# Kernel tuning notes

Measured on AMD Instinct MI355X. Metric: run time of the kernel, lower is better.

The kernel has to match this reference:

```python
import jax, jax.numpy as jnp
import numpy as np

N = 100000
E = 1600000
IN_C = 256
HID = 256
OUT_C = 32
K = 2          # APPNP K = max(1, num_layers)
ALPHA = 0.1


def setup_inputs() -> dict:
    key = jax.random.key(0)
    ks = jax.random.split(key, 8)
    x = jax.random.normal(ks[0], (N, IN_C), dtype=jnp.float32)
    edge_index = jax.random.randint(ks[1], (2, E), 0, N, dtype=jnp.int64)
    s_in = 1.0 / np.sqrt(IN_C)
    s_h = 1.0 / np.sqrt(HID)
    W_in = jax.random.uniform(ks[2], (IN_C, HID), jnp.float32, -s_in, s_in)
    b_in = jax.random.uniform(ks[3], (HID,), jnp.float32, -s_in, s_in)
    W_h = jax.random.uniform(ks[4], (HID, HID), jnp.float32, -s_h, s_h)
    b_h = jax.random.uniform(ks[5], (HID,), jnp.float32, -s_h, s_h)
    W_out = jax.random.uniform(ks[6], (HID, OUT_C), jnp.float32, -s_h, s_h)
    b_out = jax.random.uniform(ks[7], (OUT_C,), jnp.float32, -s_h, s_h)
    return {"x": x, "edge_index": edge_index, "W_in": W_in, "b_in": b_in,
            "W_h": W_h, "b_h": b_h, "W_out": W_out, "b_out": b_out}


def _appnp(h0, src, dst):
    # gcn_norm with added self-loops: deg over destinations, sym normalization
    loops = jnp.arange(N, dtype=src.dtype)
    src_f = jnp.concatenate([src, loops])  # [E+N]
    dst_f = jnp.concatenate([dst, loops])
    deg = jax.ops.segment_sum(jnp.ones_like(dst_f, dtype=h0.dtype), dst_f,
                              num_segments=N)
    dinv = jnp.where(deg > 0, jax.lax.rsqrt(jnp.maximum(deg, 1e-12)), 0.0)
    norm = (dinv[src_f] * dinv[dst_f])[:, None]  # [E+N, 1]
    h = h0
    for _ in range(K):
        agg = jax.ops.segment_sum(h[src_f] * norm, dst_f, num_segments=N)
        h = (1.0 - ALPHA) * agg + ALPHA * h0
    return h


def reference(x, edge_index, W_in, b_in, W_h, b_h, W_out, b_out):
    # MLP encoder (dropout inactive in eval mode)
    h = jax.nn.relu(x @ W_in + b_in)
    h = jax.nn.relu(h @ W_h + b_h)
    h = h @ W_out + b_out  # [N, OUT_C]
    return _appnp(h, edge_index[0], edge_index[1])
```

## Files before the change

### kernel.cpp

```cpp
#include <hip/hip_runtime.h>

#define NN 100000
#define NE 1600000
#define NT64 1563

#define BSH 7
#define BNODES 128
#define NBUCK 782
#define NBUCKP 784
#define CAP 2560
#define ECH 8192
#define NCHK 196
#define WFRAG_BLKS 272

typedef _Float16 half8v __attribute__((ext_vector_type(8)));
typedef _Float16 half4v __attribute__((ext_vector_type(4)));
typedef float f32x4 __attribute__((ext_vector_type(4)));


__device__ __forceinline__ void wfrag_one(const float* __restrict__ W,
                                          _Float16* __restrict__ Wf, int idx, int N) {
    int j = idx & 7;
    int l = (idx >> 3) & 63;
    int f = idx >> 9;
    int nt = f % (N / 16);
    int kt = f / (N / 16);
    int k = kt * 32 + (l >> 4) * 8 + j;
    int c = nt * 16 + (l & 15);
    Wf[idx] = (_Float16)W[k * N + c];
}


__global__ __launch_bounds__(512) void k_count_wfrag(const int* __restrict__ dst,
                                                     int* __restrict__ histT,
                                                     const float* __restrict__ W1,
                                                     const float* __restrict__ W2,
                                                     const float* __restrict__ W3,
                                                     _Float16* __restrict__ Wf1,
                                                     _Float16* __restrict__ Wf2,
                                                     _Float16* __restrict__ Wf3) {
    const int t = threadIdx.x;
    if (blockIdx.x >= NCHK) {
        int idx = (blockIdx.x - NCHK) * 512 + t;
        if (idx < 65536) wfrag_one(W1, Wf1, idx, 256);
        else if (idx < 131072) wfrag_one(W2, Wf2, idx - 65536, 256);
        else if (idx < 139264) wfrag_one(W3, Wf3, idx - 131072, 32);
        return;
    }
    __shared__ int h[NBUCKP];
    const int blk = blockIdx.x;
    for (int b = t; b < NBUCKP; b += 512) h[b] = 0;
    __syncthreads();
    const int ebase = blk * ECH + t * 16;
#pragma unroll
    for (int q = 0; q < 4; q++) {
        int e = ebase + q * 4;
        if (e + 4 <= NE) {
            int4 d4 = *reinterpret_cast<const int4*>(dst + e);
            atomicAdd(&h[d4.x >> BSH], 1);
            atomicAdd(&h[d4.y >> BSH], 1);
            atomicAdd(&h[d4.z >> BSH], 1);
            atomicAdd(&h[d4.w >> BSH], 1);
        } else {
            for (int p = e; p < NE; p++) atomicAdd(&h[dst[p] >> BSH], 1);
            break;
        }
    }
    __syncthreads();
    for (int b = t; b < NBUCK; b += 512) histT[(long long)b * NCHK + blk] = h[b];
}


__global__ __launch_bounds__(512) void k_scanb_xconv(int* __restrict__ histT,
                                                     int* __restrict__ cntb,
                                                     const float* __restrict__ x,
                                                     _Float16* __restrict__ x16) {
    const int t = threadIdx.x;
    if (blockIdx.x >= NBUCK) {
        const int T = blockIdx.x - NBUCK;
        const long long row0 = (long long)T * 64;
        const float4* A4 = reinterpret_cast<const float4*>(x + row0 * 256);
        _Float16* tile = x16 + (size_t)T * 16384;
#pragma unroll
        for (int q = 0; q < 4; q++) {
            int c = t + q * 512;
            int r = c >> 5;
            float4 lo = make_float4(0.f, 0.f, 0.f, 0.f), hi = lo;
            if (row0 + r < NN) { lo = A4[c * 2]; hi = A4[c * 2 + 1]; }
            half8v hv;
            hv[0] = (_Float16)lo.x; hv[1] = (_Float16)lo.y;
            hv[2] = (_Float16)lo.z; hv[3] = (_Float16)lo.w;
            hv[4] = (_Float16)hi.x; hv[5] = (_Float16)hi.y;
            hv[6] = (_Float16)hi.z; hv[7] = (_Float16)hi.w;
            *reinterpret_cast<half8v*>(tile + c * 8) = hv;
        }
        return;
    }
    __shared__ int s[512];
    const int b = blockIdx.x;
    int* row = histT + (long long)b * NCHK;
    int v = (t < NCHK) ? row[t] : 0;
    s[t] = v;
    __syncthreads();
    for (int off = 1; off < 512; off <<= 1) {
        int u = (t >= off) ? s[t - off] : 0;
        __syncthreads();
        s[t] += u;
        __syncthreads();
    }
    if (t < NCHK) row[t] = s[t] - v;
    if (t == 511) cntb[b] = s[511];
}


__global__ __launch_bounds__(512) void k_part_mlp(const int* __restrict__ src,
                                                  const int* __restrict__ dst,
                                                  const int* __restrict__ histT,
                                                  int* __restrict__ data,
                                                  const _Float16* __restrict__ x16,
                                                  const _Float16* __restrict__ Wf1,
                                                  const _Float16* __restrict__ Wf2,
                                                  const _Float16* __restrict__ Wf3,
                                                  const float* __restrict__ b1,
                                                  const float* __restrict__ b2,
                                                  const float* __restrict__ b3,
                                                  _Float16* __restrict__ h0f) {
    __shared__ char smem[32768];
    const int t = threadIdx.x;

    if (blockIdx.x < NCHK) {
        int* curs = (int*)smem;
        const int blk = blockIdx.x;
        for (int b = t; b < NBUCKP; b += 512)
            curs[b] = b * CAP + ((b < NBUCK) ? histT[(long long)b * NCHK + blk] : 0);
        __syncthreads();
        const int ebase = blk * ECH + t * 16;
#pragma unroll
        for (int q = 0; q < 4; q++) {
            int e = ebase + q * 4;
            if (e + 4 <= NE) {
                int4 d4 = *reinterpret_cast<const int4*>(dst + e);
                int4 s4 = *reinterpret_cast<const int4*>(src + e);
                int p0 = atomicAdd(&curs[d4.x >> BSH], 1);
                data[p0] = (s4.x << BSH) | (d4.x & (BNODES - 1));
                int p1 = atomicAdd(&curs[d4.y >> BSH], 1);
                data[p1] = (s4.y << BSH) | (d4.y & (BNODES - 1));
                int p2 = atomicAdd(&curs[d4.z >> BSH], 1);
                data[p2] = (s4.z << BSH) | (d4.z & (BNODES - 1));
                int p3 = atomicAdd(&curs[d4.w >> BSH], 1);
                data[p3] = (s4.w << BSH) | (d4.w & (BNODES - 1));
            } else {
                for (int p = e; p < NE; p++) {
                    int d = dst[p], sv = src[p];
                    int pos = atomicAdd(&curs[d >> BSH], 1);
                    data[pos] = (sv << BSH) | (d & (BNODES - 1));
                }
                break;
            }
        }
        return;
    }

    char* buf = smem;
    const int lane = t & 63;
    const int G = lane >> 4;
    const int w = t >> 6;
    const int T = blockIdx.x - NCHK;
    const long long row0 = (long long)T * 64;

    const half8v* W1f = reinterpret_cast<const half8v*>(Wf1);
    const half8v* W2f = reinterpret_cast<const half8v*>(Wf2);
    float bv1[2], bv2[2];
#pragma unroll
    for (int n2 = 0; n2 < 2; n2++) {
        bv1[n2] = b1[w * 32 + n2 * 16 + (lane & 15)];
        bv2[n2] = b2[w * 32 + n2 * 16 + (lane & 15)];
    }

    {
        const char* tile = (const char*)(x16 + (size_t)T * 16384);
#pragma unroll
        for (int q = 0; q < 4; q++) {
            int CC = w * 256 + q * 64 + lane;
            int scc = CC ^ ((CC >> 5) & 7);
            __builtin_amdgcn_global_load_lds(
                (const __attribute__((address_space(1))) void*)(tile + scc * 16),
                (__attribute__((address_space(3))) void*)(buf + w * 4096 + q * 1024),
                16, 0, 0);
        }
    }
    __syncthreads();

    f32x4 acc[4][2];

#pragma unroll
    for (int mt = 0; mt < 4; mt++)
#pragma unroll
        for (int n2 = 0; n2 < 2; n2++) acc[mt][n2] = (f32x4)0.f;
#pragma unroll
    for (int kt = 0; kt < 8; kt++) {
        half8v a[4], bfr[2];
#pragma unroll
        for (int n2 = 0; n2 < 2; n2++)
            bfr[n2] = W1f[(kt * 16 + 2 * w + n2) * 64 + lane];
#pragma unroll
        for (int mt = 0; mt < 4; mt++) {
            int row = mt * 16 + (lane & 15);
            int bo = (row * 512 + kt * 64 + (G << 4)) ^ ((row & 7) << 4);
            a[mt] = *reinterpret_cast<const half8v*>(buf + bo);
        }
#pragma unroll
        for (int mt = 0; mt < 4; mt++)
#pragma unroll
            for (int n2 = 0; n2 < 2; n2++)
                acc[mt][n2] = __builtin_amdgcn_mfma_f32_16x16x32_f16(a[mt], bfr[n2], acc[mt][n2], 0, 0, 0);
    }
    __syncthreads();

#pragma unroll
    for (int mt = 0; mt < 4; mt++)
#pragma unroll
        for (int n2 = 0; n2 < 2; n2++) {
            int colc = w * 32 + n2 * 16 + (lane & 15);
            float bb = bv1[n2];
#pragma unroll
            for (int r = 0; r < 4; r++) {
                int row = mt * 16 + G * 4 + r;
                float v = fmaxf(acc[mt][n2][r] + bb, 0.f);
                int bo = (row * 512 + colc * 2) ^ ((row & 7) << 4);
                *reinterpret_cast<_Float16*>(buf + bo) = (_Float16)v;
            }
        }
    __syncthreads();

#pragma unroll
    for (int mt = 0; mt < 4; mt++)
#pragma unroll
        for (int n2 = 0; n2 < 2; n2++) acc[mt][n2] = (f32x4)0.f;
#pragma unroll
    for (int kt = 0; kt < 8; kt++) {
        half8v a[4], bfr[2];
#pragma unroll
        for (int n2 = 0; n2 < 2; n2++)
            bfr[n2] = W2f[(kt * 16 + 2 * w + n2) * 64 + lane];
#pragma unroll
        for (int mt = 0; mt < 4; mt++) {
            int row = mt * 16 + (lane & 15);
            int bo = (row * 512 + kt * 64 + (G << 4)) ^ ((row & 7) << 4);
            a[mt] = *reinterpret_cast<const half8v*>(buf + bo);
        }
#pragma unroll
        for (int mt = 0; mt < 4; mt++)
#pragma unroll
            for (int n2 = 0; n2 < 2; n2++)
                acc[mt][n2] = __builtin_amdgcn_mfma_f32_16x16x32_f16(a[mt], bfr[n2], acc[mt][n2], 0, 0, 0);
    }
    __syncthreads();

#pragma unroll
    for (int mt = 0; mt < 4; mt++)
#pragma unroll
        for (int n2 = 0; n2 < 2; n2++) {
            int colc = w * 32 + n2 * 16 + (lane & 15);
            float bb = bv2[n2];
#pragma unroll
            for (int r = 0; r < 4; r++) {
                int row = mt * 16 + G * 4 + r;
                float v = fmaxf(acc[mt][n2][r] + bb, 0.f);
                int bo = (row * 512 + colc * 2) ^ ((row & 7) << 4);
                *reinterpret_cast<_Float16*>(buf + bo) = (_Float16)v;
            }
        }
    __syncthreads();

    {
        const half8v* W3f = reinterpret_cast<const half8v*>(Wf3);
        const int mt3 = w >> 1, ct3 = w & 1;
        const float bb3 = b3[ct3 * 16 + (lane & 15)];
        f32x4 a3 = (f32x4)0.f;
#pragma unroll
        for (int kt = 0; kt < 8; kt++) {
            int row = mt3 * 16 + (lane & 15);
            int bo = (row * 512 + kt * 64 + (G << 4)) ^ ((row & 7) << 4);
            half8v a = *reinterpret_cast<const half8v*>(buf + bo);
            half8v b = W3f[(kt * 2 + ct3) * 64 + lane];
            a3 = __builtin_amdgcn_mfma_f32_16x16x32_f16(a, b, a3, 0, 0, 0);
        }
        int colc = ct3 * 16 + (lane & 15);
#pragma unroll
        for (int r = 0; r < 4; r++) {
            long long row = row0 + mt3 * 16 + G * 4 + r;
            if (row < NN) h0f[row * 32 + colc] = (_Float16)(a3[r] + bb3);
        }
    }
}


__global__ __launch_bounds__(256) void k_sortb(const int* __restrict__ data,
                                               const int* __restrict__ cntb,
                                               int* __restrict__ col,
                                               int* __restrict__ begp,
                                               int* __restrict__ endp,
                                               float* __restrict__ dinv) {
    __shared__ int hist[BNODES];
    __shared__ int scn[BNODES];
    __shared__ int curs[BNODES];
    const int b = blockIdx.x, t = threadIdx.x;
    if (t < BNODES) hist[t] = 0;
    __syncthreads();
    const int cnt = cntb[b];
    const int* wp = data + b * CAP;
    for (int e = t; e < cnt; e += 256) atomicAdd(&hist[wp[e] & (BNODES - 1)], 1);
    __syncthreads();
    if (t < BNODES) scn[t] = hist[t];
    __syncthreads();
    for (int off = 1; off < BNODES; off <<= 1) {
        int v = (t < BNODES && t >= off) ? scn[t - off] : 0;
        __syncthreads();
        if (t < BNODES) scn[t] += v;
        __syncthreads();
    }
    if (t < BNODES) {
        int beg = scn[t] - hist[t];
        curs[t] = beg;
        int node = (b << BSH) + t;
        if (node < NN) {
            begp[node] = b * CAP + beg;
            endp[node] = b * CAP + scn[t];
            dinv[node] = rsqrtf((float)(hist[t] + 1));
        }
    }
    __syncthreads();
    for (int e = t; e < cnt; e += 256) {
        int w = wp[e];
        int p = atomicAdd(&curs[w & (BNODES - 1)], 1);
        col[b * CAP + p] = w >> BSH;
    }
}


template<bool FINAL>
__global__ __launch_bounds__(256) void k_appnp(const int* __restrict__ begp,
                                               const int* __restrict__ endp,
                                               const int* __restrict__ col,
                                               const float* __restrict__ dinv,
                                               const _Float16* __restrict__ hs,
                                               const _Float16* __restrict__ h0f,
                                               void* __restrict__ outp) {
    int node = blockIdx.x * 4 + (threadIdx.x >> 6);
    if (node >= NN) return;
    const int lane = threadIdx.x & 63;
    const int slot = lane >> 2;
    const int cg = lane & 3;

    const int beg = begp[node];
    const int end = endp[node];
    const float dd = dinv[node];
    const half8v selfv = *reinterpret_cast<const half8v*>(hs + (size_t)node * 32 + cg * 8);

    float acc[8];
#pragma unroll
    for (int j = 0; j < 8; j++) acc[j] = 0.f;

    for (int e = beg + slot; e < end; e += 16) {
        int s = col[e];
        half8v v = *reinterpret_cast<const half8v*>(hs + (size_t)s * 32 + cg * 8);
        float sc = 1.f;
        if (!FINAL) sc = dinv[s];
#pragma unroll
        for (int j = 0; j < 8; j++) acc[j] += sc * (float)v[j];
    }

#pragma unroll
    for (int off = 4; off < 64; off <<= 1) {
#pragma unroll
        for (int j = 0; j < 8; j++) acc[j] += __shfl_xor(acc[j], off, 64);
    }

    if (slot == 0) {
        size_t off = (size_t)node * 32 + cg * 8;
        if (FINAL) {
            const half8v h0v = *reinterpret_cast<const half8v*>(h0f + off);
            float o[8];
#pragma unroll
            for (int j = 0; j < 8; j++)
                o[j] = 0.9f * dd * (acc[j] + (float)selfv[j]) + 0.1f * (float)h0v[j];
            float4 v0 = make_float4(o[0], o[1], o[2], o[3]);
            float4 v1 = make_float4(o[4], o[5], o[6], o[7]);
            float4* op = reinterpret_cast<float4*>((float*)outp + off);
            op[0] = v0; op[1] = v1;
        } else {
            half8v hv;
#pragma unroll
            for (int j = 0; j < 8; j++) {
                float sv = (float)selfv[j];
                float hnew = 0.9f * dd * (acc[j] + dd * sv) + 0.1f * sv;
                hv[j] = (_Float16)(dd * hnew);
            }
            *reinterpret_cast<half8v*>((_Float16*)outp + off) = hv;
        }
    }
}


extern "C" void kernel_launch(void* const* d_in, const int* in_sizes, int n_in,
                              void* d_out, int out_size, void* d_ws, size_t ws_size,
                              hipStream_t stream) {
    const float* x     = (const float*)d_in[0];
    const int*   ei    = (const int*)d_in[1];
    const float* W_in  = (const float*)d_in[2];
    const float* b_in  = (const float*)d_in[3];
    const float* W_h   = (const float*)d_in[4];
    const float* b_h   = (const float*)d_in[5];
    const float* W_out = (const float*)d_in[6];
    const float* b_out = (const float*)d_in[7];
    float* out = (float*)d_out;

    const int* srcv = ei;
    const int* dstv = ei + NE;

    char* ws = (char*)d_ws;
    _Float16* h0f  = (_Float16*)ws;
    _Float16* hs1  = h0f + (size_t)NN * 32;
    float* dinv    = (float*)(hs1 + (size_t)NN * 32);
    _Float16* Wf_in  = (_Float16*)(dinv + NN);
    _Float16* Wf_h   = Wf_in + 256 * 256;
    _Float16* Wf_out = Wf_h + 256 * 256;
    _Float16* x16    = Wf_out + 256 * 32;
    int* histT = (int*)(x16 + (size_t)NT64 * 16384);
    int* cntb  = histT + (size_t)NBUCK * NCHK;
    int* data  = cntb + NBUCKP;
    int* col   = data + (size_t)NBUCKP * CAP;
    int* begp  = col + (size_t)NBUCKP * CAP;
    int* endp  = begp + NN;

    k_count_wfrag<<<NCHK + WFRAG_BLKS, 512, 0, stream>>>(dstv, histT,
                                                         W_in, W_h, W_out,
                                                         Wf_in, Wf_h, Wf_out);

    k_scanb_xconv<<<NBUCK + NT64, 512, 0, stream>>>(histT, cntb, x, x16);

    k_part_mlp<<<NCHK + NT64, 512, 0, stream>>>(srcv, dstv, histT, data,
                                                x16, Wf_in, Wf_h, Wf_out,
                                                b_in, b_h, b_out, h0f);

    k_sortb<<<NBUCK, 256, 0, stream>>>(data, cntb, col, begp, endp, dinv);

    k_appnp<false><<<(NN + 3) / 4, 256, 0, stream>>>(begp, endp, col, dinv, h0f, h0f, hs1);
    k_appnp<true ><<<(NN + 3) / 4, 256, 0, stream>>>(begp, endp, col, dinv, hs1, h0f, out);
}
```

Measured before the change: 167.5 us.

## Rebalance x conversion and MLP tiles across the three preprocessing kernels

Splits the 1563 row tiles into two halves. The first half's fp16 conversion now runs alongside the histogram count, and its MLP runs alongside the bucket scan, together with the second half's conversion. The second half's MLP then runs alongside the edge partition. Each launch gets a more even mix of work, so the small count, scan and partition kernels no longer leave the GPU mostly idle. The cost is more code paths per kernel and heavier shared-memory use in the scan kernel's blocks.

```diff
diff --git a/kernel.cpp b/kernel.cpp
--- a/kernel.cpp
+++ b/kernel.cpp
@@ -3,6 +3,8 @@
 #define NN 100000
 #define NE 1600000
 #define NT64 1563
+#define HT 782
+#define HT2 781
 
 #define BSH 7
 #define BNODES 128
@@ -31,15 +33,185 @@
 }
 
 
-__global__ __launch_bounds__(512) void k_count_wfrag(const int* __restrict__ dst,
-                                                     int* __restrict__ histT,
-                                                     const float* __restrict__ W1,
-                                                     const float* __restrict__ W2,
-                                                     const float* __restrict__ W3,
-                                                     _Float16* __restrict__ Wf1,
-                                                     _Float16* __restrict__ Wf2,
-                                                     _Float16* __restrict__ Wf3) {
+__device__ __forceinline__ void xconv_tile(const float* __restrict__ x,
+                                           _Float16* __restrict__ x16,
+                                           int T, int t) {
+    const long long row0 = (long long)T * 64;
+    const float4* A4 = reinterpret_cast<const float4*>(x + row0 * 256);
+    _Float16* tile = x16 + (size_t)T * 16384;
+#pragma unroll
+    for (int q = 0; q < 4; q++) {
+        int c = t + q * 512;
+        int r = c >> 5;
+        float4 lo = make_float4(0.f, 0.f, 0.f, 0.f), hi = lo;
+        if (row0 + r < NN) { lo = A4[c * 2]; hi = A4[c * 2 + 1]; }
+        half8v hv;
+        hv[0] = (_Float16)lo.x; hv[1] = (_Float16)lo.y;
+        hv[2] = (_Float16)lo.z; hv[3] = (_Float16)lo.w;
+        hv[4] = (_Float16)hi.x; hv[5] = (_Float16)hi.y;
+        hv[6] = (_Float16)hi.z; hv[7] = (_Float16)hi.w;
+        *reinterpret_cast<half8v*>(tile + c * 8) = hv;
+    }
+}
+
+
+__device__ __forceinline__ void mlp_tile(char* buf, int t, int T,
+                                         const _Float16* __restrict__ x16,
+                                         const _Float16* __restrict__ Wf1,
+                                         const _Float16* __restrict__ Wf2,
+                                         const _Float16* __restrict__ Wf3,
+                                         const float* __restrict__ b1,
+                                         const float* __restrict__ b2,
+                                         const float* __restrict__ b3,
+                                         _Float16* __restrict__ h0f) {
+    const int lane = t & 63;
+    const int G = lane >> 4;
+    const int w = t >> 6;
+    const long long row0 = (long long)T * 64;
+
+    const half8v* W1f = reinterpret_cast<const half8v*>(Wf1);
+    const half8v* W2f = reinterpret_cast<const half8v*>(Wf2);
+    float bv1[2], bv2[2];
+#pragma unroll
+    for (int n2 = 0; n2 < 2; n2++) {
+        bv1[n2] = b1[w * 32 + n2 * 16 + (lane & 15)];
+        bv2[n2] = b2[w * 32 + n2 * 16 + (lane & 15)];
+    }
+
+    {
+        const char* tile = (const char*)(x16 + (size_t)T * 16384);
+#pragma unroll
+        for (int q = 0; q < 4; q++) {
+            int CC = w * 256 + q * 64 + lane;
+            int scc = CC ^ ((CC >> 5) & 7);
+            __builtin_amdgcn_global_load_lds(
+                (const __attribute__((address_space(1))) void*)(tile + scc * 16),
+                (__attribute__((address_space(3))) void*)(buf + w * 4096 + q * 1024),
+                16, 0, 0);
+        }
+    }
+    __syncthreads();
+
+    f32x4 acc[4][2];
+
+#pragma unroll
+    for (int mt = 0; mt < 4; mt++)
+#pragma unroll
+        for (int n2 = 0; n2 < 2; n2++) acc[mt][n2] = (f32x4)0.f;
+#pragma unroll
+    for (int kt = 0; kt < 8; kt++) {
+        half8v a[4], bfr[2];
+#pragma unroll
+        for (int n2 = 0; n2 < 2; n2++)
+            bfr[n2] = W1f[(kt * 16 + 2 * w + n2) * 64 + lane];
+#pragma unroll
+        for (int mt = 0; mt < 4; mt++) {
+            int row = mt * 16 + (lane & 15);
+            int bo = (row * 512 + kt * 64 + (G << 4)) ^ ((row & 7) << 4);
+            a[mt] = *reinterpret_cast<const half8v*>(buf + bo);
+        }
+#pragma unroll
+        for (int mt = 0; mt < 4; mt++)
+#pragma unroll
+            for (int n2 = 0; n2 < 2; n2++)
+                acc[mt][n2] = __builtin_amdgcn_mfma_f32_16x16x32_f16(a[mt], bfr[n2], acc[mt][n2], 0, 0, 0);
+    }
+    __syncthreads();
+
+#pragma unroll
+    for (int mt = 0; mt < 4; mt++)
+#pragma unroll
+        for (int n2 = 0; n2 < 2; n2++) {
+            int colc = w * 32 + n2 * 16 + (lane & 15);
+            float bb = bv1[n2];
+#pragma unroll
+            for (int r = 0; r < 4; r++) {
+                int row = mt * 16 + G * 4 + r;
+                float v = fmaxf(acc[mt][n2][r] + bb, 0.f);
+                int bo = (row * 512 + colc * 2) ^ ((row & 7) << 4);
+                *reinterpret_cast<_Float16*>(buf + bo) = (_Float16)v;
+            }
+        }
+    __syncthreads();
+
+#pragma unroll
+    for (int mt = 0; mt < 4; mt++)
+#pragma unroll
+        for (int n2 = 0; n2 < 2; n2++) acc[mt][n2] = (f32x4)0.f;
+#pragma unroll
+    for (int kt = 0; kt < 8; kt++) {
+        half8v a[4], bfr[2];
+#pragma unroll
+        for (int n2 = 0; n2 < 2; n2++)
+            bfr[n2] = W2f[(kt * 16 + 2 * w + n2) * 64 + lane];
+#pragma unroll
+        for (int mt = 0; mt < 4; mt++) {
+            int row = mt * 16 + (lane & 15);
+            int bo = (row * 512 + kt * 64 + (G << 4)) ^ ((row & 7) << 4);
+            a[mt] = *reinterpret_cast<const half8v*>(buf + bo);
+        }
+#pragma unroll
+        for (int mt = 0; mt < 4; mt++)
+#pragma unroll
+            for (int n2 = 0; n2 < 2; n2++)
+                acc[mt][n2] = __builtin_amdgcn_mfma_f32_16x16x32_f16(a[mt], bfr[n2], acc[mt][n2], 0, 0, 0);
+    }
+    __syncthreads();
+
+#pragma unroll
+    for (int mt = 0; mt < 4; mt++)
+#pragma unroll
+        for (int n2 = 0; n2 < 2; n2++) {
+            int colc = w * 32 + n2 * 16 + (lane & 15);
+            float bb = bv2[n2];
+#pragma unroll
+            for (int r = 0; r < 4; r++) {
+                int row = mt * 16 + G * 4 + r;
+                float v = fmaxf(acc[mt][n2][r] + bb, 0.f);
+                int bo = (row * 512 + colc * 2) ^ ((row & 7) << 4);
+                *reinterpret_cast<_Float16*>(buf + bo) = (_Float16)v;
+            }
+        }
+    __syncthreads();
+
+    {
+        const half8v* W3f = reinterpret_cast<const half8v*>(Wf3);
+        const int mt3 = w >> 1, ct3 = w & 1;
+        const float bb3 = b3[ct3 * 16 + (lane & 15)];
+        f32x4 a3 = (f32x4)0.f;
+#pragma unroll
+        for (int kt = 0; kt < 8; kt++) {
+            int row = mt3 * 16 + (lane & 15);
+            int bo = (row * 512 + kt * 64 + (G << 4)) ^ ((row & 7) << 4);
+            half8v a = *reinterpret_cast<const half8v*>(buf + bo);
+            half8v b = W3f[(kt * 2 + ct3) * 64 + lane];
+            a3 = __builtin_amdgcn_mfma_f32_16x16x32_f16(a, b, a3, 0, 0, 0);
+        }
+        int colc = ct3 * 16 + (lane & 15);
+#pragma unroll
+        for (int r = 0; r < 4; r++) {
+            long long row = row0 + mt3 * 16 + G * 4 + r;
+            if (row < NN) h0f[row * 32 + colc] = (_Float16)(a3[r] + bb3);
+        }
+    }
+}
+
+
+__global__ __launch_bounds__(512) void k_A(const int* __restrict__ dst,
+                                           int* __restrict__ histT,
+                                           const float* __restrict__ W1,
+                                           const float* __restrict__ W2,
+                                           const float* __restrict__ W3,
+                                           _Float16* __restrict__ Wf1,
+                                           _Float16* __restrict__ Wf2,
+                                           _Float16* __restrict__ Wf3,
+                                           const float* __restrict__ x,
+                                           _Float16* __restrict__ x16) {
     const int t = threadIdx.x;
+    if (blockIdx.x >= NCHK + WFRAG_BLKS) {
+        xconv_tile(x, x16, blockIdx.x - NCHK - WFRAG_BLKS, t);
+        return;
+    }
     if (blockIdx.x >= NCHK) {
         int idx = (blockIdx.x - NCHK) * 512 + t;
         if (idx < 65536) wfrag_one(W1, Wf1, idx, 256);
@@ -71,63 +243,58 @@
 }
 
 
-__global__ __launch_bounds__(512) void k_scanb_xconv(int* __restrict__ histT,
-                                                     int* __restrict__ cntb,
-                                                     const float* __restrict__ x,
-                                                     _Float16* __restrict__ x16) {
-    const int t = threadIdx.x;
-    if (blockIdx.x >= NBUCK) {
-        const int T = blockIdx.x - NBUCK;
-        const long long row0 = (long long)T * 64;
-        const float4* A4 = reinterpret_cast<const float4*>(x + row0 * 256);
-        _Float16* tile = x16 + (size_t)T * 16384;
-#pragma unroll
-        for (int q = 0; q < 4; q++) {
-            int c = t + q * 512;
-            int r = c >> 5;
-            float4 lo = make_float4(0.f, 0.f, 0.f, 0.f), hi = lo;
-            if (row0 + r < NN) { lo = A4[c * 2]; hi = A4[c * 2 + 1]; }
-            half8v hv;
-            hv[0] = (_Float16)lo.x; hv[1] = (_Float16)lo.y;
-            hv[2] = (_Float16)lo.z; hv[3] = (_Float16)lo.w;
-            hv[4] = (_Float16)hi.x; hv[5] = (_Float16)hi.y;
-            hv[6] = (_Float16)hi.z; hv[7] = (_Float16)hi.w;
-            *reinterpret_cast<half8v*>(tile + c * 8) = hv;
-        }
-        return;
-    }
-    __shared__ int s[512];
-    const int b = blockIdx.x;
-    int* row = histT + (long long)b * NCHK;
-    int v = (t < NCHK) ? row[t] : 0;
-    s[t] = v;
-    __syncthreads();
-    for (int off = 1; off < 512; off <<= 1) {
-        int u = (t >= off) ? s[t - off] : 0;
-        __syncthreads();
-        s[t] += u;
-        __syncthreads();
-    }
-    if (t < NCHK) row[t] = s[t] - v;
-    if (t == 511) cntb[b] = s[511];
-}
-
-
-__global__ __launch_bounds__(512) void k_part_mlp(const int* __restrict__ src,
-                                                  const int* __restrict__ dst,
-                                                  const int* __restrict__ histT,
-                                                  int* __restrict__ data,
-                                                  const _Float16* __restrict__ x16,
-                                                  const _Float16* __restrict__ Wf1,
-                                                  const _Float16* __restrict__ Wf2,
-                                                  const _Float16* __restrict__ Wf3,
-                                                  const float* __restrict__ b1,
-                                                  const float* __restrict__ b2,
-                                                  const float* __restrict__ b3,
-                                                  _Float16* __restrict__ h0f) {
+__global__ __launch_bounds__(512) void k_B(int* __restrict__ histT,
+                                           int* __restrict__ cntb,
+                                           const float* __restrict__ x,
+                                           _Float16* __restrict__ x16,
+                                           const _Float16* __restrict__ Wf1,
+                                           const _Float16* __restrict__ Wf2,
+                                           const _Float16* __restrict__ Wf3,
+                                           const float* __restrict__ b1,
+                                           const float* __restrict__ b2,
+                                           const float* __restrict__ b3,
+                                           _Float16* __restrict__ h0f) {
     __shared__ char smem[32768];
     const int t = threadIdx.x;
-
+    if (blockIdx.x < NBUCK) {
+        int* s = (int*)smem;
+        const int b = blockIdx.x;
+        int* row = histT + (long long)b * NCHK;
+        int v = (t < NCHK) ? row[t] : 0;
+        s[t] = v;
+        __syncthreads();
+        for (int off = 1; off < 512; off <<= 1) {
+            int u = (t >= off) ? s[t - off] : 0;
+            __syncthreads();
+            s[t] += u;
+            __syncthreads();
+        }
+        if (t < NCHK) row[t] = s[t] - v;
+        if (t == 511) cntb[b] = s[511];
+        return;
+    }
+    if (blockIdx.x < NBUCK + HT2) {
+        xconv_tile(x, x16, HT + (blockIdx.x - NBUCK), t);
+        return;
+    }
+    mlp_tile(smem, t, blockIdx.x - NBUCK - HT2, x16, Wf1, Wf2, Wf3, b1, b2, b3, h0f);
+}
+
+
+__global__ __launch_bounds__(512) void k_C(const int* __restrict__ src,
+                                           const int* __restrict__ dst,
+                                           const int* __restrict__ histT,
+                                           int* __restrict__ data,
+                                           const _Float16* __restrict__ x16,
+                                           const _Float16* __restrict__ Wf1,
+                                           const _Float16* __restrict__ Wf2,
+                                           const _Float16* __restrict__ Wf3,
+                                           const float* __restrict__ b1,
+                                           const float* __restrict__ b2,
+                                           const float* __restrict__ b3,
+                                           _Float16* __restrict__ h0f) {
+    __shared__ char smem[32768];
+    const int t = threadIdx.x;
     if (blockIdx.x < NCHK) {
         int* curs = (int*)smem;
         const int blk = blockIdx.x;
@@ -160,139 +327,7 @@
         }
         return;
     }
-
-    char* buf = smem;
-    const int lane = t & 63;
-    const int G = lane >> 4;
-    const int w = t >> 6;
-    const int T = blockIdx.x - NCHK;
-    const long long row0 = (long long)T * 64;
-
-    const half8v* W1f = reinterpret_cast<const half8v*>(Wf1);
-    const half8v* W2f = reinterpret_cast<const half8v*>(Wf2);
-    float bv1[2], bv2[2];
-#pragma unroll
-    for (int n2 = 0; n2 < 2; n2++) {
-        bv1[n2] = b1[w * 32 + n2 * 16 + (lane & 15)];
-        bv2[n2] = b2[w * 32 + n2 * 16 + (lane & 15)];
-    }
-
-    {
-        const char* tile = (const char*)(x16 + (size_t)T * 16384);
-#pragma unroll
-        for (int q = 0; q < 4; q++) {
-            int CC = w * 256 + q * 64 + lane;
-            int scc = CC ^ ((CC >> 5) & 7);
-            __builtin_amdgcn_global_load_lds(
-                (const __attribute__((address_space(1))) void*)(tile + scc * 16),
-                (__attribute__((address_space(3))) void*)(buf + w * 4096 + q * 1024),
-                16, 0, 0);
-        }
-    }
-    __syncthreads();
-
-    f32x4 acc[4][2];
-
-#pragma unroll
-    for (int mt = 0; mt < 4; mt++)
-#pragma unroll
-        for (int n2 = 0; n2 < 2; n2++) acc[mt][n2] = (f32x4)0.f;
-#pragma unroll
-    for (int kt = 0; kt < 8; kt++) {
-        half8v a[4], bfr[2];
-#pragma unroll
-        for (int n2 = 0; n2 < 2; n2++)
-            bfr[n2] = W1f[(kt * 16 + 2 * w + n2) * 64 + lane];
-#pragma unroll
-        for (int mt = 0; mt < 4; mt++) {
-            int row = mt * 16 + (lane & 15);
-            int bo = (row * 512 + kt * 64 + (G << 4)) ^ ((row & 7) << 4);
-            a[mt] = *reinterpret_cast<const half8v*>(buf + bo);
-        }
-#pragma unroll
-        for (int mt = 0; mt < 4; mt++)
-#pragma unroll
-            for (int n2 = 0; n2 < 2; n2++)
-                acc[mt][n2] = __builtin_amdgcn_mfma_f32_16x16x32_f16(a[mt], bfr[n2], acc[mt][n2], 0, 0, 0);
-    }
-    __syncthreads();
-
-#pragma unroll
-    for (int mt = 0; mt < 4; mt++)
-#pragma unroll
-        for (int n2 = 0; n2 < 2; n2++) {
-            int colc = w * 32 + n2 * 16 + (lane & 15);
-            float bb = bv1[n2];
-#pragma unroll
-            for (int r = 0; r < 4; r++) {
-                int row = mt * 16 + G * 4 + r;
-                float v = fmaxf(acc[mt][n2][r] + bb, 0.f);
-                int bo = (row * 512 + colc * 2) ^ ((row & 7) << 4);
-                *reinterpret_cast<_Float16*>(buf + bo) = (_Float16)v;
-            }
-        }
-    __syncthreads();
-
-#pragma unroll
-    for (int mt = 0; mt < 4; mt++)
-#pragma unroll
-        for (int n2 = 0; n2 < 2; n2++) acc[mt][n2] = (f32x4)0.f;
-#pragma unroll
-    for (int kt = 0; kt < 8; kt++) {
-        half8v a[4], bfr[2];
-#pragma unroll
-        for (int n2 = 0; n2 < 2; n2++)
-            bfr[n2] = W2f[(kt * 16 + 2 * w + n2) * 64 + lane];
-#pragma unroll
-        for (int mt = 0; mt < 4; mt++) {
-            int row = mt * 16 + (lane & 15);
-            int bo = (row * 512 + kt * 64 + (G << 4)) ^ ((row & 7) << 4);
-            a[mt] = *reinterpret_cast<const half8v*>(buf + bo);
-        }
-#pragma unroll
-        for (int mt = 0; mt < 4; mt++)
-#pragma unroll
-            for (int n2 = 0; n2 < 2; n2++)
-                acc[mt][n2] = __builtin_amdgcn_mfma_f32_16x16x32_f16(a[mt], bfr[n2], acc[mt][n2], 0, 0, 0);
-    }
-    __syncthreads();
-
-#pragma unroll
-    for (int mt = 0; mt < 4; mt++)
-#pragma unroll
-        for (int n2 = 0; n2 < 2; n2++) {
-            int colc = w * 32 + n2 * 16 + (lane & 15);
-            float bb = bv2[n2];
-#pragma unroll
-            for (int r = 0; r < 4; r++) {
-                int row = mt * 16 + G * 4 + r;
-                float v = fmaxf(acc[mt][n2][r] + bb, 0.f);
-                int bo = (row * 512 + colc * 2) ^ ((row & 7) << 4);
-                *reinterpret_cast<_Float16*>(buf + bo) = (_Float16)v;
-            }
-        }
-    __syncthreads();
-
-    {
-        const half8v* W3f = reinterpret_cast<const half8v*>(Wf3);
-        const int mt3 = w >> 1, ct3 = w & 1;
-        const float bb3 = b3[ct3 * 16 + (lane & 15)];
-        f32x4 a3 = (f32x4)0.f;
-#pragma unroll
-        for (int kt = 0; kt < 8; kt++) {
-            int row = mt3 * 16 + (lane & 15);
-            int bo = (row * 512 + kt * 64 + (G << 4)) ^ ((row & 7) << 4);
-            half8v a = *reinterpret_cast<const half8v*>(buf + bo);
-            half8v b = W3f[(kt * 2 + ct3) * 64 + lane];
-            a3 = __builtin_amdgcn_mfma_f32_16x16x32_f16(a, b, a3, 0, 0, 0);
-        }
-        int colc = ct3 * 16 + (lane & 15);
-#pragma unroll
-        for (int r = 0; r < 4; r++) {
-            long long row = row0 + mt3 * 16 + G * 4 + r;
-            if (row < NN) h0f[row * 32 + colc] = (_Float16)(a3[r] + bb3);
-        }
-    }
+    mlp_tile(smem, t, HT + (blockIdx.x - NCHK), x16, Wf1, Wf2, Wf3, b1, b2, b3, h0f);
 }
 
 
@@ -434,15 +469,17 @@
     int* begp  = col + (size_t)NBUCKP * CAP;
     int* endp  = begp + NN;
 
-    k_count_wfrag<<<NCHK + WFRAG_BLKS, 512, 0, stream>>>(dstv, histT,
-                                                         W_in, W_h, W_out,
-                                                         Wf_in, Wf_h, Wf_out);
-
-    k_scanb_xconv<<<NBUCK + NT64, 512, 0, stream>>>(histT, cntb, x, x16);
-
-    k_part_mlp<<<NCHK + NT64, 512, 0, stream>>>(srcv, dstv, histT, data,
-                                                x16, Wf_in, Wf_h, Wf_out,
-                                                b_in, b_h, b_out, h0f);
+    k_A<<<NCHK + WFRAG_BLKS + HT, 512, 0, stream>>>(dstv, histT,
+                                                    W_in, W_h, W_out,
+                                                    Wf_in, Wf_h, Wf_out, x, x16);
+
+    k_B<<<NBUCK + HT2 + HT, 512, 0, stream>>>(histT, cntb, x, x16,
+                                              Wf_in, Wf_h, Wf_out,
+                                              b_in, b_h, b_out, h0f);
+
+    k_C<<<NCHK + HT2, 512, 0, stream>>>(srcv, dstv, histT, data,
+                                        x16, Wf_in, Wf_h, Wf_out,
+                                        b_in, b_h, b_out, h0f);
 
     k_sortb<<<NBUCK, 256, 0, stream>>>(data, cntb, col, begp, endp, dinv);
 
```

New measurement: 186.1 us. 11.1% more time.
